# Kernel optimization log

Measured on AMD Instinct MI355X. Metric: run time of the kernel, lower is better.

## Reference

```python
import jax, jax.numpy as jnp
import numpy as np
from jax import lax

B = 16384
BN_EPS = 1e-5


def setup_inputs() -> dict:
    key = jax.random.key(0)
    ks = jax.random.split(key, 6)
    x = jax.random.normal(ks[0], (B, 1, 28, 28), jnp.float32)
    conv_w = jax.random.normal(ks[1], (4, 1, 3, 3), jnp.float32) * 0.2
    bn_gamma = jnp.ones((4,), jnp.float32)
    bn_beta = jnp.zeros((4,), jnp.float32)
    bn_mean = jnp.zeros((4,), jnp.float32)
    bn_var = jnp.ones((4,), jnp.float32)
    var_params = jax.random.normal(ks[2], (4,), jnp.float32)
    lin_w = jax.random.normal(ks[3], (10, 784), jnp.float32) * 0.03
    lin_b = jnp.zeros((10,), jnp.float32)
    return {"x": x, "conv_w": conv_w, "bn_gamma": bn_gamma, "bn_beta": bn_beta,
            "bn_mean": bn_mean, "bn_var": bn_var, "var_params": var_params,
            "lin_w": lin_w, "lin_b": lin_b}


def _ry_w0(s, theta):
    # apply RY(theta) to wire 0 (axis -2) of real state s[..., 2, 2]
    c, si = jnp.cos(theta * 0.5), jnp.sin(theta * 0.5)
    R = jnp.stack([jnp.stack([c, -si]), jnp.stack([si, c])])
    return jnp.einsum('ij,...jk->...ik', R, s)


def _ry_w1(s, theta):
    # apply RY(theta) to wire 1 (axis -1)
    c, si = jnp.cos(theta * 0.5), jnp.sin(theta * 0.5)
    R = jnp.stack([jnp.stack([c, -si]), jnp.stack([si, c])])
    return jnp.einsum('ij,...kj->...ki', R, s)


def _quantum_features(img, v):
    # img: [B, 28, 28] -> features [B, 196*4] (patch-major, 4 expvals each)
    b = img.shape[0]
    p = img.reshape(b, 14, 2, 14, 2).transpose(0, 1, 3, 2, 4)  # [B,14,14,2,2]
    # encoding RYs on same wire compose: angles a = p0+p2 (wire0), b = p1+p3 (wire1)
    ha = (p[..., 0, 0] + p[..., 1, 0]) * 0.5
    hb = (p[..., 0, 1] + p[..., 1, 1]) * 0.5
    w0 = jnp.stack([jnp.cos(ha), jnp.sin(ha)], axis=-1)
    w1 = jnp.stack([jnp.cos(hb), jnp.sin(hb)], axis=-1)
    s = w0[..., :, None] * w1[..., None, :]  # real statevector [B,14,14,2,2]
    # CNOT(control=0, target=1): flip wire1 where wire0 == 1
    s = jnp.stack([s[..., 0, :], s[..., 1, ::-1]], axis=-2)
    s = _ry_w0(s, v[0])
    s = _ry_w1(s, v[1])
    # CNOT(control=1, target=0): flip wire0 where wire1 == 1
    s = jnp.stack([s[..., :, 0], s[..., ::-1, 1]], axis=-1)
    s = _ry_w0(s, v[2])
    s = _ry_w1(s, v[3])
    z0 = jnp.sum(s[..., 0, :] ** 2 - s[..., 1, :] ** 2, axis=-1)
    z1 = jnp.sum(s[..., :, 0] ** 2 - s[..., :, 1] ** 2, axis=-1)
    x0 = 2.0 * jnp.sum(s[..., 0, :] * s[..., 1, :], axis=-1)
    x1 = 2.0 * jnp.sum(s[..., :, 0] * s[..., :, 1], axis=-1)
    return jnp.stack([z0, z1, x0, x1], axis=-1).reshape(b, -1)  # [B,784]


def reference(x, conv_w, bn_gamma, bn_beta, bn_mean, bn_var, var_params, lin_w, lin_b):
    b = x.shape[0]
    # classical branch: conv(s=2,p=1) -> BN (eval) -> ReLU -> flatten
    h = lax.conv_general_dilated(x, conv_w, window_strides=(2, 2),
                                 padding=((1, 1), (1, 1)))  # [B,4,14,14]
    inv = bn_gamma / jnp.sqrt(bn_var + BN_EPS)
    h = h * inv[None, :, None, None] + (bn_beta - bn_mean * inv)[None, :, None, None]
    h = jnp.maximum(h, 0.0)
    cls_out = h.reshape(b, -1)  # [B,784]
    # quantum branch over 2x2 patches
    q_out = _quantum_features(x[:, 0], var_params)  # [B,784]
    fused = cls_out + q_out
    logits = fused @ lin_w.T + lin_b
    return jax.nn.log_softmax(logits, axis=-1)
```

## Files before the change

### kernel.cpp

```cpp
#include <hip/hip_runtime.h>
#include <math.h>


#define NW 4
#define SCLS_STRIDE 794

typedef __fp16 h2 __attribute__((ext_vector_type(2)));
typedef __fp16 h4 __attribute__((ext_vector_type(4)));

#if __has_builtin(__builtin_amdgcn_fdot2)
#define FDOT2(a, b, c) __builtin_amdgcn_fdot2((a), (b), (c), false)
#else
__device__ __forceinline__ float FDOT2(h2 a, h2 b, float c) {
    return (float)a.x * (float)b.x + (float)a.y * (float)b.y + c;
}
#endif

__device__ __forceinline__ float2 red32x2(float x) {
    int v;
    v = __builtin_amdgcn_update_dpp(0, __float_as_int(x), 0x111, 0xf, 0xf, true); x += __int_as_float(v);
    v = __builtin_amdgcn_update_dpp(0, __float_as_int(x), 0x112, 0xf, 0xf, true); x += __int_as_float(v);
    v = __builtin_amdgcn_update_dpp(0, __float_as_int(x), 0x114, 0xf, 0xf, true); x += __int_as_float(v);
    v = __builtin_amdgcn_update_dpp(0, __float_as_int(x), 0x118, 0xf, 0xf, true); x += __int_as_float(v);
    v = __builtin_amdgcn_update_dpp(0, __float_as_int(x), 0x142, 0xa, 0xf, true); x += __int_as_float(v);
    float2 r;
    r.x = __int_as_float(__builtin_amdgcn_readlane(__float_as_int(x), 31));
    r.y = __int_as_float(__builtin_amdgcn_readlane(__float_as_int(x), 63));
    return r;
}

__global__ __launch_bounds__(256, 4)
void quanv_fused(const float* __restrict__ x,
                 const float* __restrict__ conv_w,
                 const float* __restrict__ bn_gamma,
                 const float* __restrict__ bn_beta,
                 const float* __restrict__ bn_mean,
                 const float* __restrict__ bn_var,
                 const float* __restrict__ var_params,
                 const float* __restrict__ lin_w,
                 const float* __restrict__ lin_b,
                 float* __restrict__ out, int B)
{
    __shared__ __align__(16) __fp16 lwh[7840];
    __shared__ __align__(16) __fp16 sclsAll[NW * 2 * SCLS_STRIDE];

    const int tid  = threadIdx.x;
    const int wave = tid >> 6;
    const int lane = tid & 63;
    const int half = lane >> 5;
    const int l32  = lane & 31;

    const int s  = blockIdx.x * (NW * 2) + wave * 2 + half;
    const int sc = (s < B) ? s : (B - 1);
    const float* xs = x + (size_t)sc * 784;
    __fp16* myscls = &sclsAll[(wave * 2 + half) * SCLS_STRIDE];

    {
        const float4* src = (const float4*)lin_w;
        #pragma unroll
        for (int t = 0; t < 8; ++t) {
            int i = tid + t * 256;
            if (i < 1960) {
                float4 v = src[i];
                h2 a = __builtin_amdgcn_cvt_pkrtz(v.x, v.y);
                h2 b = __builtin_amdgcn_cvt_pkrtz(v.z, v.w);
                h4 w4 = { a.x, a.y, b.x, b.y };
                *(h4*)&lwh[4 * i] = w4;
            }
        }
    }

    float w[36];
    #pragma unroll
    for (int k = 0; k < 36; ++k) w[k] = conv_w[k];
    float inv[4], addc[4];
    #pragma unroll
    for (int c = 0; c < 4; ++c) {
        float iv = bn_gamma[c] * rsqrtf(bn_var[c] + 1e-5f);
        inv[c]  = iv;
        addc[c] = bn_beta[c] - bn_mean[c] * iv;
    }
    float cv[4], sv[4];
    #pragma unroll
    for (int k = 0; k < 4; ++k) __sincosf(var_params[k] * 0.5f, &sv[k], &cv[k]);

    h2 qh[7][2];
    #pragma unroll
    for (int t = 0; t < 7; ++t) {
        int p = l32 + 32 * t;
        bool act = (p < 196);
        int pc = act ? p : 195;
        unsigned i = (unsigned)pc / 14u;
        int j = pc - (int)i * 14;
        int omid = (int)(2 * i) * 28 + 2 * j;

        float2 Rm = *(const float2*)(xs + omid);
        float2 Rb = *(const float2*)(xs + omid + 28);
        int ot = omid - 28; ot = (ot > 0) ? ot : 0;
        float2 Rt = *(const float2*)(xs + ot);
        int olt = omid - 30; olt = (olt > 0) ? olt : 0;
        float2 Lt = *(const float2*)(xs + olt);
        int olm = omid - 2; olm = (olm > 0) ? olm : 0;
        float2 Lm = *(const float2*)(xs + olm);
        float2 Lb = *(const float2*)(xs + olm + 28);

        float mt = (i > 0) ? 1.f : 0.f;
        float ml = (j > 0) ? 1.f : 0.f;
        float a00 = Lt.y * (mt * ml), a01 = Rt.x * mt, a02 = Rt.y * mt;
        float a10 = Lm.y * ml,        a11 = Rm.x,      a12 = Rm.y;
        float a20 = Lb.y * ml,        a21 = Rb.x,      a22 = Rb.y;

        if (act) {
            #pragma unroll
            for (int c = 0; c < 4; ++c) {
                float h = w[c*9+0]*a00 + w[c*9+1]*a01 + w[c*9+2]*a02
                        + w[c*9+3]*a10 + w[c*9+4]*a11 + w[c*9+5]*a12
                        + w[c*9+6]*a20 + w[c*9+7]*a21 + w[c*9+8]*a22;
                h = h * inv[c] + addc[c];
                myscls[c * 196 + pc] = (__fp16)fmaxf(h, 0.f);
            }
        }

        float ha = 0.5f * (a11 + a21);
        float hb = 0.5f * (a12 + a22);
        float c0, s0, c1, s1;
        __sincosf(ha, &s0, &c0);
        __sincosf(hb, &s1, &c1);
        float m00 = c0*c1, m01 = c0*s1;
        float m10 = s0*s1, m11 = s0*c1;
        float t00 = cv[0]*m00 - sv[0]*m10, t01 = cv[0]*m01 - sv[0]*m11;
        float t10 = sv[0]*m00 + cv[0]*m10, t11 = sv[0]*m01 + cv[0]*m11;
        float u00 = cv[1]*t00 - sv[1]*t01, u01 = sv[1]*t00 + cv[1]*t01;
        float u10 = cv[1]*t10 - sv[1]*t11, u11 = sv[1]*t10 + cv[1]*t11;
        float tmp = u01; u01 = u11; u11 = tmp;
        float p00 = cv[2]*u00 - sv[2]*u10, p01 = cv[2]*u01 - sv[2]*u11;
        float p10 = sv[2]*u00 + cv[2]*u10, p11 = sv[2]*u01 + cv[2]*u11;
        float q00 = cv[3]*p00 - sv[3]*p01, q01 = sv[3]*p00 + cv[3]*p01;
        float q10 = cv[3]*p10 - sv[3]*p11, q11 = sv[3]*p10 + cv[3]*p11;

        float z0 = q00*q00 + q01*q01 - q10*q10 - q11*q11;
        float z1 = q00*q00 + q10*q10 - q01*q01 - q11*q11;
        float x0 = 2.f * (q00*q10 + q01*q11);
        float x1 = 2.f * (q00*q01 + q10*q11);
        qh[t][0] = __builtin_amdgcn_cvt_pkrtz(z0, z1);
        qh[t][1] = __builtin_amdgcn_cvt_pkrtz(x0, x1);
    }

    __syncthreads();

    float ps[10];
    #pragma unroll
    for (int o = 0; o < 10; ++o) ps[o] = 0.f;

    const h2 hz = { (__fp16)0.f, (__fp16)0.f };
    #pragma unroll
    for (int t = 0; t < 7; ++t) {
        int p = l32 + 32 * t;
        bool act = (p < 196);
        int pc = act ? p : 195;
        h2 c0 = *(const h2*)&myscls[4 * pc];
        h2 c1 = *(const h2*)&myscls[4 * pc + 2];
        h2 f0 = c0 + qh[t][0];
        h2 f1 = c1 + qh[t][1];
        f0 = act ? f0 : hz;
        f1 = act ? f1 : hz;
        const __fp16* wbase = &lwh[4 * pc];
        #pragma unroll
        for (int o = 0; o < 10; ++o) {
            h4 wv = *(const h4*)&wbase[o * 784];
            h2 wlo = __builtin_shufflevector(wv, wv, 0, 1);
            h2 whi = __builtin_shufflevector(wv, wv, 2, 3);
            ps[o] = FDOT2(f0, wlo, ps[o]);
            ps[o] = FDOT2(f1, whi, ps[o]);
        }
    }

    float lg[10];
    #pragma unroll
    for (int o = 0; o < 10; ++o) {
        float2 r = red32x2(ps[o]);
        lg[o] = (half ? r.y : r.x) + lin_b[o];
    }

    float mx = lg[0];
    #pragma unroll
    for (int o = 1; o < 10; ++o) mx = fmaxf(mx, lg[o]);
    float se = 0.f;
    #pragma unroll
    for (int o = 0; o < 10; ++o) se += __expf(lg[o] - mx);
    float ls = __logf(se);

    int o32 = l32;
    if (o32 < 10 && s < B) {
        float v = lg[0];
        #pragma unroll
        for (int o = 1; o < 10; ++o) v = (o32 == o) ? lg[o] : v;
        out[(size_t)s * 10 + o32] = v - mx - ls;
    }
}

extern "C" void kernel_launch(void* const* d_in, const int* in_sizes, int n_in,
                              void* d_out, int out_size, void* d_ws, size_t ws_size,
                              hipStream_t stream) {
    const float* x          = (const float*)d_in[0];
    const float* conv_w     = (const float*)d_in[1];
    const float* bn_gamma   = (const float*)d_in[2];
    const float* bn_beta    = (const float*)d_in[3];
    const float* bn_mean    = (const float*)d_in[4];
    const float* bn_var     = (const float*)d_in[5];
    const float* var_params = (const float*)d_in[6];
    const float* lin_w      = (const float*)d_in[7];
    const float* lin_b      = (const float*)d_in[8];
    float* out = (float*)d_out;

    const int B = in_sizes[0] / 784;
    const int blocks = (B + NW * 2 - 1) / (NW * 2);
    quanv_fused<<<blocks, 256, 0, stream>>>(x, conv_w, bn_gamma, bn_beta, bn_mean,
                                            bn_var, var_params, lin_w, lin_b, out, B);
}
```

Baseline: 110.7 us.

## Precompute fp16 linear weights in a pre-kernel and read them from global memory

Adds a small kernel that converts lin_w to fp16 once into workspace, so each block no longer converts the weights and stages them into LDS. The fused kernel now reads the fp16 weights straight from global/L2, removes the block-wide barrier in favour of a per-wave LDS waitcnt, folds the BN scale into the conv weights, and raises launch_bounds occupancy to 5. This cuts LDS use and per-block setup in exchange for an extra launch and repeated global weight loads, which depend on cache hits.

```diff
diff --git a/kernel.cpp b/kernel.cpp
--- a/kernel.cpp
+++ b/kernel.cpp
@@ -8,13 +8,8 @@
 typedef __fp16 h2 __attribute__((ext_vector_type(2)));
 typedef __fp16 h4 __attribute__((ext_vector_type(4)));
 
-#if __has_builtin(__builtin_amdgcn_fdot2)
 #define FDOT2(a, b, c) __builtin_amdgcn_fdot2((a), (b), (c), false)
-#else
-__device__ __forceinline__ float FDOT2(h2 a, h2 b, float c) {
-    return (float)a.x * (float)b.x + (float)a.y * (float)b.y + c;
-}
-#endif
+#define PK(a, b) __builtin_amdgcn_cvt_pkrtz((a), (b))
 
 __device__ __forceinline__ float2 red32x2(float x) {
     int v;
@@ -29,7 +24,18 @@
     return r;
 }
 
-__global__ __launch_bounds__(256, 4)
+__global__ void w_to_f16(const float* __restrict__ lin_w, __fp16* __restrict__ w16) {
+    int i = blockIdx.x * 256 + threadIdx.x;
+    if (i < 1960) {
+        float4 v = ((const float4*)lin_w)[i];
+        h2 a = PK(v.x, v.y);
+        h2 b = PK(v.z, v.w);
+        h4 w4 = { a.x, a.y, b.x, b.y };
+        *(h4*)&w16[4 * i] = w4;
+    }
+}
+
+__global__ __launch_bounds__(256, 5)
 void quanv_fused(const float* __restrict__ x,
                  const float* __restrict__ conv_w,
                  const float* __restrict__ bn_gamma,
@@ -37,11 +43,10 @@
                  const float* __restrict__ bn_mean,
                  const float* __restrict__ bn_var,
                  const float* __restrict__ var_params,
-                 const float* __restrict__ lin_w,
+                 const __fp16* __restrict__ w16,
                  const float* __restrict__ lin_b,
                  float* __restrict__ out, int B)
 {
-    __shared__ __align__(16) __fp16 lwh[7840];
     __shared__ __align__(16) __fp16 sclsAll[NW * 2 * SCLS_STRIDE];
 
     const int tid  = threadIdx.x;
@@ -55,30 +60,13 @@
     const float* xs = x + (size_t)sc * 784;
     __fp16* myscls = &sclsAll[(wave * 2 + half) * SCLS_STRIDE];
 
-    {
-        const float4* src = (const float4*)lin_w;
-        #pragma unroll
-        for (int t = 0; t < 8; ++t) {
-            int i = tid + t * 256;
-            if (i < 1960) {
-                float4 v = src[i];
-                h2 a = __builtin_amdgcn_cvt_pkrtz(v.x, v.y);
-                h2 b = __builtin_amdgcn_cvt_pkrtz(v.z, v.w);
-                h4 w4 = { a.x, a.y, b.x, b.y };
-                *(h4*)&lwh[4 * i] = w4;
-            }
-        }
-    }
-
-    float w[36];
-    #pragma unroll
-    for (int k = 0; k < 36; ++k) w[k] = conv_w[k];
-    float inv[4], addc[4];
+    float w[36], addc[4];
     #pragma unroll
     for (int c = 0; c < 4; ++c) {
         float iv = bn_gamma[c] * rsqrtf(bn_var[c] + 1e-5f);
-        inv[c]  = iv;
         addc[c] = bn_beta[c] - bn_mean[c] * iv;
+        #pragma unroll
+        for (int k = 0; k < 9; ++k) w[c * 9 + k] = conv_w[c * 9 + k] * iv;
     }
     float cv[4], sv[4];
     #pragma unroll
@@ -113,10 +101,10 @@
         if (act) {
             #pragma unroll
             for (int c = 0; c < 4; ++c) {
-                float h = w[c*9+0]*a00 + w[c*9+1]*a01 + w[c*9+2]*a02
+                float h = addc[c]
+                        + w[c*9+0]*a00 + w[c*9+1]*a01 + w[c*9+2]*a02
                         + w[c*9+3]*a10 + w[c*9+4]*a11 + w[c*9+5]*a12
                         + w[c*9+6]*a20 + w[c*9+7]*a21 + w[c*9+8]*a22;
-                h = h * inv[c] + addc[c];
                 myscls[c * 196 + pc] = (__fp16)fmaxf(h, 0.f);
             }
         }
@@ -142,32 +130,33 @@
         float z1 = q00*q00 + q10*q10 - q01*q01 - q11*q11;
         float x0 = 2.f * (q00*q10 + q01*q11);
         float x1 = 2.f * (q00*q01 + q10*q11);
-        qh[t][0] = __builtin_amdgcn_cvt_pkrtz(z0, z1);
-        qh[t][1] = __builtin_amdgcn_cvt_pkrtz(x0, x1);
-    }
-
-    __syncthreads();
+        qh[t][0] = PK(z0, z1);
+        qh[t][1] = PK(x0, x1);
+    }
+
+    asm volatile("s_waitcnt lgkmcnt(0)" ::: "memory");
 
     float ps[10];
     #pragma unroll
     for (int o = 0; o < 10; ++o) ps[o] = 0.f;
 
+    const h4* gw = (const h4*)w16;
     const h2 hz = { (__fp16)0.f, (__fp16)0.f };
     #pragma unroll
     for (int t = 0; t < 7; ++t) {
         int p = l32 + 32 * t;
         bool act = (p < 196);
         int pc = act ? p : 195;
-        h2 c0 = *(const h2*)&myscls[4 * pc];
-        h2 c1 = *(const h2*)&myscls[4 * pc + 2];
+        h4 cl4 = *(const h4*)&myscls[4 * pc];
+        h2 c0 = __builtin_shufflevector(cl4, cl4, 0, 1);
+        h2 c1 = __builtin_shufflevector(cl4, cl4, 2, 3);
         h2 f0 = c0 + qh[t][0];
         h2 f1 = c1 + qh[t][1];
         f0 = act ? f0 : hz;
         f1 = act ? f1 : hz;
-        const __fp16* wbase = &lwh[4 * pc];
         #pragma unroll
         for (int o = 0; o < 10; ++o) {
-            h4 wv = *(const h4*)&wbase[o * 784];
+            h4 wv = gw[o * 196 + pc];
             h2 wlo = __builtin_shufflevector(wv, wv, 0, 1);
             h2 whi = __builtin_shufflevector(wv, wv, 2, 3);
             ps[o] = FDOT2(f0, wlo, ps[o]);
@@ -190,12 +179,11 @@
     for (int o = 0; o < 10; ++o) se += __expf(lg[o] - mx);
     float ls = __logf(se);
 
-    int o32 = l32;
-    if (o32 < 10 && s < B) {
+    if (l32 < 10 && s < B) {
         float v = lg[0];
         #pragma unroll
-        for (int o = 1; o < 10; ++o) v = (o32 == o) ? lg[o] : v;
-        out[(size_t)s * 10 + o32] = v - mx - ls;
+        for (int o = 1; o < 10; ++o) v = (l32 == o) ? lg[o] : v;
+        out[(size_t)s * 10 + l32] = v - mx - ls;
     }
 }
 
@@ -212,9 +200,13 @@
     const float* lin_w      = (const float*)d_in[7];
     const float* lin_b      = (const float*)d_in[8];
     float* out = (float*)d_out;
+    __fp16* w16 = (__fp16*)d_ws;
 
     const int B = in_sizes[0] / 784;
+
+    w_to_f16<<<8, 256, 0, stream>>>(lin_w, w16);
+
     const int blocks = (B + NW * 2 - 1) / (NW * 2);
     quanv_fused<<<blocks, 256, 0, stream>>>(x, conv_w, bn_gamma, bn_beta, bn_mean,
-                                            bn_var, var_params, lin_w, lin_b, out, B);
-}
+                                            bn_var, var_params, w16, lin_b, out, B);
+}
```

After: 126.5 us. 14.3% more time.
